# Kernel tuning notes

Measured on AMD Instinct MI355X. Metric: run time of the kernel, lower is better.

The kernel has to match this reference:

```python
import jax, jax.numpy as jnp
import numpy as np

EPS = 1e-5

def layer_norm(x, g, b):
    m = jnp.mean(x, axis=-1, keepdims=True)
    v = jnp.var(x, axis=-1, keepdims=True)
    return (x - m) / jnp.sqrt(v + EPS) * g + b


def setup_inputs() -> dict:
    key = jax.random.key(0)
    ks = jax.random.split(key, 12)
    B, L, D = 4, 4096, 512
    DF = 2 * D  # dim * dim_ff_scale
    inp = {
        "x": jax.random.normal(ks[0], (B, L, D), dtype=jnp.float32),
        "hidden_real": jax.random.normal(ks[1], (B, D), dtype=jnp.float32),
        "hidden_imag": jax.random.normal(ks[2], (B, D), dtype=jnp.float32),
        # SpiralConv complex params (real/imag parts), as torch.randn cfloat
        "phazor_re": jax.random.normal(ks[3], (D,), dtype=jnp.float32),
        "phazor_im": jax.random.normal(ks[4], (D,), dtype=jnp.float32),
        "pinit_re": jax.random.normal(ks[5], (D,), dtype=jnp.float32),
        "pinit_im": jax.random.normal(ks[6], (D,), dtype=jnp.float32),
        # shared LayerNorm params
        "ln_g": jnp.ones((D,), dtype=jnp.float32),
        "ln_b": jnp.zeros((D,), dtype=jnp.float32),
        # FFN params
        "w1": jax.random.normal(ks[7], (D, DF), dtype=jnp.float32) * (1.0 / np.sqrt(D)),
        "b1": jnp.zeros((DF,), dtype=jnp.float32),
        "w2": jax.random.normal(ks[8], (DF, D), dtype=jnp.float32) * (1.0 / np.sqrt(DF)),
        "b2": jnp.zeros((D,), dtype=jnp.float32),
    }
    return inp


def reference(x, hidden_real, hidden_imag, phazor_re, phazor_im,
              pinit_re, pinit_im, ln_g, ln_b, w1, b1, w2, b2):
    B, L, D = x.shape
    p = jax.lax.complex(phazor_re, phazor_im)
    pinit = jax.lax.complex(pinit_re, pinit_im)
    hidden_last = jax.lax.complex(hidden_real, hidden_imag)

    # phazor = p/|p| * exp(-|p|)  (unit direction, decaying magnitude)
    absp = jnp.abs(p)
    phazor = p / absp * jnp.exp(-absp)

    # phazor_progression[t, d] = phazor[d] ** t
    t = jnp.arange(L, dtype=jnp.float32)
    prog = jnp.exp(t[:, None] * jnp.log(phazor)[None, :])  # [L, D] complex
    filt = prog * pinit[None, :]                            # [L, D]

    x_res = x
    xn = layer_norm(x, ln_g, ln_b)

    # FFT long convolution along sequence, zero-padded to 2L (linear conv)
    filt_fft = jnp.fft.fft(filt, n=2 * L, axis=0)           # [2L, D]
    x_fft = jnp.fft.fft(xn, n=2 * L, axis=1)                # [B, 2L, D]
    conv = jnp.fft.ifft(filt_fft[None, :, :] * x_fft, axis=1)[:, :L, :]

    hidden = conv + hidden_last[:, None, :] * prog[None, :, :] * phazor[None, None, :]

    y = hidden.real + x_res
    yn = layer_norm(y, ln_g, ln_b)
    h = yn @ w1 + b1
    h = h * jax.nn.sigmoid(h)  # SiLU; dropout=0 (eval) is identity
    out = h @ w2 + b2 + y
    return out, hidden
```

## Files before the change

kernel.cpp:

```cpp
#include <hip/hip_runtime.h>
#include <hip/hip_bf16.h>
#include <math.h>

#define BB 4
#define LL 4096
#define DD 512
#define DF 1024
#define CHUNKS 64
#define LC 64
#define HALF_ROWS 8192

typedef __bf16 bf16x8 __attribute__((ext_vector_type(8)));
typedef float f32x4 __attribute__((ext_vector_type(4)));

__device__ inline void get_phazor(const float* __restrict__ pre, const float* __restrict__ pim,
                                  int d, float& ar, float& ai) {
    float pr = pre[d], pi = pim[d];
    float ab = sqrtf(pr * pr + pi * pi);
    float sc = expf(-ab) / ab;
    ar = pr * sc;
    ai = pi * sc;
}

__global__ __launch_bounds__(256) void k_wt(const float* __restrict__ w1, const float* __restrict__ w2,
                                            __bf16* __restrict__ w1t, __bf16* __restrict__ w2t) {
    __shared__ float tile[32][33];
    const float* src;
    __bf16* dst;
    int R, C;
    if (blockIdx.y == 0) { src = w1; dst = w1t; R = DD; C = DF; }
    else                 { src = w2; dst = w2t; R = DF; C = DD; }
    int ntx = C / 32;
    int c0 = (blockIdx.x % ntx) * 32, r0 = (blockIdx.x / ntx) * 32;
    int tx = threadIdx.x & 31, ty = threadIdx.x >> 5;
#pragma unroll
    for (int i = 0; i < 32; i += 8)
        tile[ty + i][tx] = src[(size_t)(r0 + ty + i) * C + c0 + tx];
    __syncthreads();
#pragma unroll
    for (int i = 0; i < 32; i += 8)
        dst[(size_t)(c0 + ty + i) * R + r0 + tx] = (__bf16)tile[tx][ty + i];
}

__global__ __launch_bounds__(256) void k_xstats(const float* __restrict__ x, float* __restrict__ xstats) {
    int wave = threadIdx.x >> 6, lane = threadIdx.x & 63;
    size_t row = (size_t)blockIdx.x * 4 + wave;
    const float4* xr = reinterpret_cast<const float4*>(x + row * DD) + lane * 2;
    float4 a = xr[0], b = xr[1];
    float s = a.x + a.y + a.z + a.w + b.x + b.y + b.z + b.w;
    float q = a.x * a.x + a.y * a.y + a.z * a.z + a.w * a.w +
              b.x * b.x + b.y * b.y + b.z * b.z + b.w * b.w;
#pragma unroll
    for (int off = 32; off; off >>= 1) {
        s += __shfl_down(s, off);
        q += __shfl_down(q, off);
    }
    if (lane == 0) {
        float m = s * (1.0f / DD);
        float v = q * (1.0f / DD) - m * m;
        xstats[row * 2 + 0] = m;
        xstats[row * 2 + 1] = rsqrtf(v + 1e-5f);
    }
}

__global__ __launch_bounds__(512) void k_scan_partial(
    const float* __restrict__ x, const float* __restrict__ xstats,
    const float* __restrict__ pre, const float* __restrict__ pim,
    const float* __restrict__ pinr, const float* __restrict__ pini,
    const float* __restrict__ g, const float* __restrict__ bvec,
    float* __restrict__ carry) {
    int d = threadIdx.x;
    int c = blockIdx.x % CHUNKS, b = blockIdx.x / CHUNKS;
    float ar, ai;
    get_phazor(pre, pim, d, ar, ai);
    float pr = pinr[d], pi = pini[d];
    float gd = g[d], bd = bvec[d];
    float hr = 0.f, hi = 0.f;
    int l0 = c * LC;
    const float* xp = x + ((size_t)b * LL + l0) * DD + d;
    const float* st = xstats + ((size_t)b * LL + l0) * 2;
    for (int i = 0; i < LC; i++) {
        float m = st[2 * i], r = st[2 * i + 1];
        float xn = (xp[(size_t)i * DD] - m) * r * gd + bd;
        float ur = pr * xn, ui = pi * xn;
        float t = ar * hr - ai * hi + ur;
        hi = ar * hi + ai * hr + ui;
        hr = t;
    }
    size_t idx = ((size_t)blockIdx.x * DD + d) * 2;
    carry[idx] = hr;
    carry[idx + 1] = hi;
}

__global__ __launch_bounds__(512) void k_chunk_scan(
    const float* __restrict__ hr0, const float* __restrict__ hi0,
    const float* __restrict__ pre, const float* __restrict__ pim,
    const float* __restrict__ carry, float* __restrict__ carry_in) {
    int d = threadIdx.x, b = blockIdx.x;
    float ar, ai;
    get_phazor(pre, pim, d, ar, ai);
    float sr = ar, si = ai;
#pragma unroll
    for (int i = 0; i < 6; i++) {
        float t = sr * sr - si * si;
        si = 2.f * sr * si;
        sr = t;
    }
    float cr = hr0[b * DD + d], ci = hi0[b * DD + d];
    for (int k = 0; k < CHUNKS; k++) {
        size_t idx = (((size_t)b * CHUNKS + k) * DD + d) * 2;
        carry_in[idx] = cr;
        carry_in[idx + 1] = ci;
        float tr = carry[idx], ti = carry[idx + 1];
        float t = sr * cr - si * ci + tr;
        ci = sr * ci + si * cr + ti;
        cr = t;
    }
}

template <int MODE>
__global__ __launch_bounds__(512) void k_scan_out(
    const float* __restrict__ x, const float* __restrict__ xstats,
    const float* __restrict__ pre, const float* __restrict__ pim,
    const float* __restrict__ pinr, const float* __restrict__ pini,
    const float* __restrict__ g, const float* __restrict__ bvec,
    const float* __restrict__ carry_in,
    float* __restrict__ out_y, float* __restrict__ hid) {
    int d = threadIdx.x;
    int c = blockIdx.x % CHUNKS, b = blockIdx.x / CHUNKS;
    float ar, ai;
    get_phazor(pre, pim, d, ar, ai);
    float pr = pinr[d], pi = pini[d];
    float gd = g[d], bd = bvec[d];
    size_t cidx = ((size_t)blockIdx.x * DD + d) * 2;
    float hr = carry_in[cidx], hi = carry_in[cidx + 1];
    int l0 = c * LC;
    const float* xp = x + ((size_t)b * LL + l0) * DD + d;
    const float* st = xstats + ((size_t)b * LL + l0) * 2;
    for (int i = 0; i < LC; i++) {
        float m = st[2 * i], r = st[2 * i + 1];
        float xv = xp[(size_t)i * DD];
        float xn = (xv - m) * r * gd + bd;
        float ur = pr * xn, ui = pi * xn;
        float t = ar * hr - ai * hi + ur;
        hi = ar * hi + ai * hr + ui;
        hr = t;
        size_t row = (size_t)b * LL + l0 + i;
        if constexpr (MODE == 0) {
            out_y[row * DD + d] = hr + xv;
        } else if constexpr (MODE == 1) {
            hid[row * DD + d] = hr;
        } else if constexpr (MODE == 2) {
            reinterpret_cast<float2*>(hid)[row * DD + d] = make_float2(hr, hi);
        } else {
            out_y[row * DD + d] = hr + xv;
            hid[row * DD + d] = hr;
        }
    }
}

__global__ __launch_bounds__(256) void k_ynorm(const float* __restrict__ y,
                                               const float* __restrict__ g, const float* __restrict__ bvec,
                                               __bf16* __restrict__ yn) {
    int wave = threadIdx.x >> 6, lane = threadIdx.x & 63;
    size_t row = (size_t)blockIdx.x * 4 + wave;
    const float4* yr = reinterpret_cast<const float4*>(y + row * DD) + lane * 2;
    float4 a = yr[0], b = yr[1];
    float s = a.x + a.y + a.z + a.w + b.x + b.y + b.z + b.w;
    float q = a.x * a.x + a.y * a.y + a.z * a.z + a.w * a.w +
              b.x * b.x + b.y * b.y + b.z * b.z + b.w * b.w;
#pragma unroll
    for (int off = 32; off; off >>= 1) {
        s += __shfl_xor(s, off);
        q += __shfl_xor(q, off);
    }
    float m = s * (1.0f / DD);
    float r = rsqrtf(q * (1.0f / DD) - m * m + 1e-5f);
    int dbase = lane * 8;
    const float4* gp = reinterpret_cast<const float4*>(g + dbase);
    const float4* bp = reinterpret_cast<const float4*>(bvec + dbase);
    float4 g0 = gp[0], g1 = gp[1], b0 = bp[0], b1 = bp[1];
    bf16x8 o;
    o[0] = (__bf16)((a.x - m) * r * g0.x + b0.x);
    o[1] = (__bf16)((a.y - m) * r * g0.y + b0.y);
    o[2] = (__bf16)((a.z - m) * r * g0.z + b0.z);
    o[3] = (__bf16)((a.w - m) * r * g0.w + b0.w);
    o[4] = (__bf16)((b.x - m) * r * g1.x + b1.x);
    o[5] = (__bf16)((b.y - m) * r * g1.y + b1.y);
    o[6] = (__bf16)((b.z - m) * r * g1.z + b1.z);
    o[7] = (__bf16)((b.w - m) * r * g1.w + b1.w);
    *reinterpret_cast<bf16x8*>(yn + row * DD + dbase) = o;
}

template <int KDIM, int NDIM, int EPI>
__global__ __launch_bounds__(256) void k_gemm(
    const __bf16* __restrict__ A, const __bf16* __restrict__ Bt,
    const float* __restrict__ bias, const float* __restrict__ yadd,
    float* __restrict__ outf, __bf16* __restrict__ outb) {
    __shared__ __align__(16) __bf16 As[128 * 32];
    __shared__ __align__(16) __bf16 Bs[128 * 32];
    constexpr int NT = NDIM / 128;
    int nwg = gridDim.x;
    int bid = blockIdx.x;
    int swz = (bid & 7) * (nwg >> 3) + (bid >> 3);
    int m0 = (swz / NT) * 128;
    int n0 = (swz % NT) * 128;
    int tid = threadIdx.x;
    int wave = tid >> 6, lane = tid & 63;

    f32x4 acc[4][4] = {};

    int wm = (wave & 1) * 64, wn = (wave >> 1) * 64;
    int fr = lane & 15;
    int kk = (lane >> 4) * 8;

    for (int k0 = 0; k0 < KDIM; k0 += 32) {
        __syncthreads();
#pragma unroll
        for (int i = 0; i < 2; i++) {
            int c = tid + i * 256;
            int row = c >> 2, kq = c & 3;
            const __bf16* ga = A + (size_t)(m0 + row) * KDIM + k0 + kq * 8;
            const __bf16* gb = Bt + (size_t)(n0 + row) * KDIM + k0 + kq * 8;
            __bf16* la = As + (size_t)(i * 256 + wave * 64) * 8;
            __bf16* lb = Bs + (size_t)(i * 256 + wave * 64) * 8;
            __builtin_amdgcn_global_load_lds((const __attribute__((address_space(1))) unsigned int*)ga,
                                             (__attribute__((address_space(3))) unsigned int*)la, 16, 0, 0);
            __builtin_amdgcn_global_load_lds((const __attribute__((address_space(1))) unsigned int*)gb,
                                             (__attribute__((address_space(3))) unsigned int*)lb, 16, 0, 0);
        }
        __syncthreads();
        bf16x8 af[4], bfv[4];
#pragma unroll
        for (int mi = 0; mi < 4; mi++)
            af[mi] = *reinterpret_cast<const bf16x8*>(As + (wm + mi * 16 + fr) * 32 + kk);
#pragma unroll
        for (int ni = 0; ni < 4; ni++)
            bfv[ni] = *reinterpret_cast<const bf16x8*>(Bs + (wn + ni * 16 + fr) * 32 + kk);
#pragma unroll
        for (int mi = 0; mi < 4; mi++)
#pragma unroll
            for (int ni = 0; ni < 4; ni++)
                acc[mi][ni] = __builtin_amdgcn_mfma_f32_16x16x32_bf16(af[mi], bfv[ni], acc[mi][ni], 0, 0, 0);
    }

    int orow = (lane >> 4) * 4;
    int ocol = lane & 15;
#pragma unroll
    for (int mi = 0; mi < 4; mi++) {
#pragma unroll
        for (int ni = 0; ni < 4; ni++) {
            int gr = m0 + wm + mi * 16 + orow;
            int gc = n0 + wn + ni * 16 + ocol;
            float bv = bias[gc];
#pragma unroll
            for (int j = 0; j < 4; j++) {
                float v = acc[mi][ni][j] + bv;
                size_t idx = (size_t)(gr + j) * NDIM + gc;
                if constexpr (EPI == 1) {
                    float sv = v / (1.0f + __expf(-v));
                    outb[idx] = (__bf16)sv;
                } else {
                    outf[idx] = v + yadd[idx];
                }
            }
        }
    }
}

extern "C" void kernel_launch(void* const* d_in, const int* in_sizes, int n_in,
                              void* d_out, int out_size, void* d_ws, size_t ws_size,
                              hipStream_t stream) {
    const float* x = (const float*)d_in[0];
    const float* hr0 = (const float*)d_in[1];
    const float* hi0 = (const float*)d_in[2];
    const float* pre = (const float*)d_in[3];
    const float* pim = (const float*)d_in[4];
    const float* pinr = (const float*)d_in[5];
    const float* pini = (const float*)d_in[6];
    const float* lng = (const float*)d_in[7];
    const float* lnb = (const float*)d_in[8];
    const float* w1 = (const float*)d_in[9];
    const float* b1 = (const float*)d_in[10];
    const float* w2 = (const float*)d_in[11];
    const float* b2 = (const float*)d_in[12];

    const size_t n = (size_t)BB * LL * DD;
    float* outp = (float*)d_out;
    char* hidbase = (char*)d_out + n * 4;
    float* hidp = (float*)hidbase;
    bool interleaved = (out_size >= (int)(3 * n));

    char* ws = (char*)d_ws;
    float* xstats = (float*)ws;      ws += (size_t)BB * LL * 2 * 4;
    float* carry = (float*)ws;       ws += (size_t)BB * CHUNKS * DD * 8;
    float* carry_in = (float*)ws;    ws += (size_t)BB * CHUNKS * DD * 8;
    __bf16* w1t = (__bf16*)ws;       ws += (size_t)DD * DF * 2;
    __bf16* w2t = (__bf16*)ws;       ws += (size_t)DF * DD * 2;
    char* ws_big = ws;
    const size_t SMALL = (size_t)(128 + 1024 + 1024 + 1024 + 1024) * 1024;
    const size_t NEED_FULL = SMALL + ((size_t)48 << 20);
    const size_t NEED_HALF = SMALL + ((size_t)24 << 20);

    k_wt<<<dim3((DD / 32) * (DF / 32), 2), 256, 0, stream>>>(w1, w2, w1t, w2t);
    k_xstats<<<(BB * LL) / 4, 256, 0, stream>>>(x, xstats);
    k_scan_partial<<<BB * CHUNKS, 512, 0, stream>>>(x, xstats, pre, pim, pinr, pini, lng, lnb, carry);
    k_chunk_scan<<<BB, 512, 0, stream>>>(hr0, hi0, pre, pim, carry, carry_in);

    if (!interleaved && ws_size >= NEED_FULL) {
        __bf16* yn = (__bf16*)ws_big;
        __bf16* h1 = (__bf16*)(ws_big + ((size_t)16 << 20));
        k_scan_out<3><<<BB * CHUNKS, 512, 0, stream>>>(x, xstats, pre, pim, pinr, pini, lng, lnb,
                                                       carry_in, outp, hidp);
        k_ynorm<<<(BB * LL) / 4, 256, 0, stream>>>(outp, lng, lnb, yn);
        k_gemm<DD, DF, 1><<<(BB * LL / 128) * (DF / 128), 256, 0, stream>>>(
            yn, w1t, b1, nullptr, nullptr, h1);
        k_gemm<DF, DD, 2><<<(BB * LL / 128) * (DD / 128), 256, 0, stream>>>(
            h1, w2t, b2, outp, outp, nullptr);
    } else if (!interleaved && ws_size >= NEED_HALF) {
        __bf16* yn_h = (__bf16*)ws_big;
        __bf16* h1_h = (__bf16*)(ws_big + ((size_t)8 << 20));
        k_scan_out<3><<<BB * CHUNKS, 512, 0, stream>>>(x, xstats, pre, pim, pinr, pini, lng, lnb,
                                                       carry_in, outp, hidp);
        for (int h = 0; h < 2; h++) {
            float* yh = outp + (size_t)h * HALF_ROWS * DD;
            k_ynorm<<<HALF_ROWS / 4, 256, 0, stream>>>(yh, lng, lnb, yn_h);
            k_gemm<DD, DF, 1><<<(HALF_ROWS / 128) * (DF / 128), 256, 0, stream>>>(
                yn_h, w1t, b1, nullptr, nullptr, h1_h);
            k_gemm<DF, DD, 2><<<(HALF_ROWS / 128) * (DD / 128), 256, 0, stream>>>(
                h1_h, w2t, b2, yh, yh, nullptr);
        }
    } else {
        __bf16* yn_h = (__bf16*)hidbase;
        __bf16* h1_h = (__bf16*)(hidbase + ((size_t)8 << 20));
        k_scan_out<0><<<BB * CHUNKS, 512, 0, stream>>>(x, xstats, pre, pim, pinr, pini, lng, lnb,
                                                       carry_in, outp, nullptr);
        for (int h = 0; h < 2; h++) {
            float* yh = outp + (size_t)h * HALF_ROWS * DD;
            k_ynorm<<<HALF_ROWS / 4, 256, 0, stream>>>(yh, lng, lnb, yn_h);
            k_gemm<DD, DF, 1><<<(HALF_ROWS / 128) * (DF / 128), 256, 0, stream>>>(
                yn_h, w1t, b1, nullptr, nullptr, h1_h);
            k_gemm<DF, DD, 2><<<(HALF_ROWS / 128) * (DD / 128), 256, 0, stream>>>(
                h1_h, w2t, b2, yh, yh, nullptr);
        }
        if (interleaved) {
            k_scan_out<2><<<BB * CHUNKS, 512, 0, stream>>>(x, xstats, pre, pim, pinr, pini, lng, lnb,
                                                           carry_in, nullptr, hidp);
        } else {
            k_scan_out<1><<<BB * CHUNKS, 512, 0, stream>>>(x, xstats, pre, pim, pinr, pini, lng, lnb,
                                                           carry_in, nullptr, hidp);
        }
    }
}
```

Before: 119.6 us.

## Double-buffer GEMM LDS tiles with K=64 steps and XOR-swizzled layout

The bf16 MFMA GEMM now uses two LDS buffers so the async global-to-LDS load of the next K tile is issued before computing on the current one, which overlaps memory latency with MFMA work. The K step grows from 32 to 64, halving the number of barriers. An XOR swizzle on the 16-byte column chunks is meant to avoid LDS bank conflicts on the fragment reads. In exchange LDS use rises to 64 KB per block, which may reduce occupancy.

Result: slower. 125.7 us (+5.1%).

```diff
diff --git a/kernel.cpp b/kernel.cpp
--- a/kernel.cpp
+++ b/kernel.cpp
@@ -197,8 +197,8 @@
     const __bf16* __restrict__ A, const __bf16* __restrict__ Bt,
     const float* __restrict__ bias, const float* __restrict__ yadd,
     float* __restrict__ outf, __bf16* __restrict__ outb) {
-    __shared__ __align__(16) __bf16 As[128 * 32];
-    __shared__ __align__(16) __bf16 Bs[128 * 32];
+    __shared__ __align__(16) __bf16 As[2][128 * 64];
+    __shared__ __align__(16) __bf16 Bs[2][128 * 64];
     constexpr int NT = NDIM / 128;
     int nwg = gridDim.x;
     int bid = blockIdx.x;
@@ -212,37 +212,65 @@
 
     int wm = (wave & 1) * 64, wn = (wave >> 1) * 64;
     int fr = lane & 15;
-    int kk = (lane >> 4) * 8;
-
-    for (int k0 = 0; k0 < KDIM; k0 += 32) {
+    int qbase = lane >> 4;
+
+    int c_ = tid;
+
+#define STAGE(buf, k0)                                                                              \
+    {                                                                                               \
+        _Pragma("unroll")                                                                           \
+        for (int i = 0; i < 4; i++) {                                                               \
+            int c = c_ + i * 256;                                                                   \
+            int row = c >> 3, kq = c & 7;                                                           \
+            int kqg = kq ^ (row & 7);                                                               \
+            const __bf16* ga = A + (size_t)(m0 + row) * KDIM + (k0) + kqg * 8;                      \
+            const __bf16* gb = Bt + (size_t)(n0 + row) * KDIM + (k0) + kqg * 8;                     \
+            __bf16* la = &As[buf][(size_t)(i * 256 + wave * 64) * 8];                               \
+            __bf16* lb = &Bs[buf][(size_t)(i * 256 + wave * 64) * 8];                               \
+            __builtin_amdgcn_global_load_lds((const __attribute__((address_space(1))) unsigned int*)ga, \
+                                             (__attribute__((address_space(3))) unsigned int*)la, 16, 0, 0); \
+            __builtin_amdgcn_global_load_lds((const __attribute__((address_space(1))) unsigned int*)gb, \
+                                             (__attribute__((address_space(3))) unsigned int*)lb, 16, 0, 0); \
+        }                                                                                           \
+    }
+
+#define COMPUTE(buf)                                                                                \
+    {                                                                                               \
+        _Pragma("unroll")                                                                           \
+        for (int ks = 0; ks < 2; ks++) {                                                            \
+            int q = ks * 4 + qbase;                                                                 \
+            bf16x8 af[4], bfv[4];                                                                   \
+            _Pragma("unroll")                                                                       \
+            for (int mi = 0; mi < 4; mi++) {                                                        \
+                int R = wm + mi * 16 + fr;                                                          \
+                af[mi] = *reinterpret_cast<const bf16x8*>(&As[buf][R * 64 + ((q ^ (R & 7)) << 3)]); \
+            }                                                                                       \
+            _Pragma("unroll")                                                                       \
+            for (int ni = 0; ni < 4; ni++) {                                                        \
+                int R = wn + ni * 16 + fr;                                                          \
+                bfv[ni] = *reinterpret_cast<const bf16x8*>(&Bs[buf][R * 64 + ((q ^ (R & 7)) << 3)]);\
+            }                                                                                       \
+            _Pragma("unroll")                                                                       \
+            for (int mi = 0; mi < 4; mi++)                                                          \
+                _Pragma("unroll")                                                                   \
+                for (int ni = 0; ni < 4; ni++)                                                      \
+                    acc[mi][ni] = __builtin_amdgcn_mfma_f32_16x16x32_bf16(af[mi], bfv[ni],          \
+                                                                          acc[mi][ni], 0, 0, 0);    \
+        }                                                                                           \
+    }
+
+    STAGE(0, 0);
+    __syncthreads();
+    int cur = 0;
+    for (int k0 = 64; k0 < KDIM; k0 += 64) {
+        STAGE(cur ^ 1, k0);
+        COMPUTE(cur);
         __syncthreads();
-#pragma unroll
-        for (int i = 0; i < 2; i++) {
-            int c = tid + i * 256;
-            int row = c >> 2, kq = c & 3;
-            const __bf16* ga = A + (size_t)(m0 + row) * KDIM + k0 + kq * 8;
-            const __bf16* gb = Bt + (size_t)(n0 + row) * KDIM + k0 + kq * 8;
-            __bf16* la = As + (size_t)(i * 256 + wave * 64) * 8;
-            __bf16* lb = Bs + (size_t)(i * 256 + wave * 64) * 8;
-            __builtin_amdgcn_global_load_lds((const __attribute__((address_space(1))) unsigned int*)ga,
-                                             (__attribute__((address_space(3))) unsigned int*)la, 16, 0, 0);
-            __builtin_amdgcn_global_load_lds((const __attribute__((address_space(1))) unsigned int*)gb,
-                                             (__attribute__((address_space(3))) unsigned int*)lb, 16, 0, 0);
-        }
-        __syncthreads();
-        bf16x8 af[4], bfv[4];
-#pragma unroll
-        for (int mi = 0; mi < 4; mi++)
-            af[mi] = *reinterpret_cast<const bf16x8*>(As + (wm + mi * 16 + fr) * 32 + kk);
-#pragma unroll
-        for (int ni = 0; ni < 4; ni++)
-            bfv[ni] = *reinterpret_cast<const bf16x8*>(Bs + (wn + ni * 16 + fr) * 32 + kk);
-#pragma unroll
-        for (int mi = 0; mi < 4; mi++)
-#pragma unroll
-            for (int ni = 0; ni < 4; ni++)
-                acc[mi][ni] = __builtin_amdgcn_mfma_f32_16x16x32_bf16(af[mi], bfv[ni], acc[mi][ni], 0, 0, 0);
-    }
+        cur ^= 1;
+    }
+    COMPUTE(cur);
+#undef STAGE
+#undef COMPUTE
 
     int orow = (lane >> 4) * 4;
     int ocol = lane & 15;
```
